# Performance work log

Measured on AMD Instinct MI355X. Metric: run time of the kernel, lower is better.

## Reference

```python
import jax, jax.numpy as jnp
import numpy as np

EMBED_DIM = 1024
NUM_HEADS = 8
HEAD_DIM = EMBED_DIM // NUM_HEADS


def setup_inputs() -> dict:
    key = jax.random.key(0)
    k1, k2, k3, k4, k5 = jax.random.split(key, 5)
    B, N, D = 4, 2048, EMBED_DIM
    scale = 1.0 / np.sqrt(D)
    return {
        "representation": jax.random.normal(k1, (B, N, D), dtype=jnp.float32),
        "W_qkv": jax.random.normal(k2, (D, 3 * D), dtype=jnp.float32) * scale,
        "b_qkv": jnp.zeros((3 * D,), dtype=jnp.float32),
        "W_proj": jax.random.normal(k3, (D, D), dtype=jnp.float32) * scale,
        "b_proj": jnp.zeros((D,), dtype=jnp.float32),
    }


def reference(representation, W_qkv, b_qkv, W_proj, b_proj):
    B, N, D = representation.shape
    H, Hd = NUM_HEADS, HEAD_DIM
    qkv = jnp.einsum("bnd,de->bne", representation, W_qkv) + b_qkv  # [B,N,3D]
    q, k, v = jnp.split(qkv, 3, axis=-1)
    # [B,N,D] -> [B,H,N,Hd]
    split_heads = lambda x: x.reshape(B, N, H, Hd).transpose(0, 2, 1, 3)
    q, k, v = split_heads(q), split_heads(k), split_heads(v)
    dots = jnp.einsum("bhqd,bhkd->bhqk", q, k) * (Hd ** -0.5)  # [B,H,N,N]
    attn = jax.nn.softmax(dots, axis=-1)
    out = jnp.einsum("bhqk,bhkd->bhqd", attn, v)
    out = out.transpose(0, 2, 1, 3).reshape(B, N, D)  # merge heads
    return jnp.einsum("bnd,de->bne", out, W_proj) + b_proj
```

## Files before the change

kernel.cpp:

```cpp
#include <hip/hip_runtime.h>
#include <hip/hip_bf16.h>
#include <cstdint>

typedef unsigned short u16;
typedef __attribute__((ext_vector_type(8))) short short8;
typedef __attribute__((ext_vector_type(4))) float f32x4;
typedef __attribute__((ext_vector_type(4))) unsigned short u16x4;
typedef __attribute__((ext_vector_type(4))) unsigned int u32x4;

#define NSEQ 2048
#define DMODEL 1024
#define NH 8
#define HD 128
#define KDIM 1024
#define QSCALE (0.08838834764831845f * 1.4426950408889634f)

__device__ __forceinline__ u16 f2b(float f) {
  __hip_bfloat16 h = __float2bfloat16(f);
  union { __hip_bfloat16 h; u16 u; } cv; cv.h = h; return cv.u;
}
__device__ __forceinline__ f32x4 zero4() { f32x4 z = {0.f, 0.f, 0.f, 0.f}; return z; }

__device__ __forceinline__ void gload_lds16(const u16* g, u16* l) {
  __builtin_amdgcn_global_load_lds(
      (__attribute__((address_space(1))) void*)g,
      (__attribute__((address_space(3))) void*)l, 16, 0, 0);
}

__device__ __forceinline__ int LK(int r) {
  return (r & 0x23) | ((r & 0x0C) << 1) | ((r & 0x10) >> 2);
}

__global__ void cvt_f32_bf16(const float* __restrict__ in, u16* __restrict__ out) {
  const size_t i = ((size_t)blockIdx.x * 256 + threadIdx.x) * 8;
  f32x4 a = *(const f32x4*)&in[i];
  f32x4 b = *(const f32x4*)&in[i + 4];
  short8 o;
#pragma unroll
  for (int j = 0; j < 4; ++j) { o[j] = (short)f2b(a[j]); o[4 + j] = (short)f2b(b[j]); }
  *(short8*)&out[i] = o;
}

__global__ void transpose_k(const float* __restrict__ in, u16* __restrict__ out,
                            int R, int C) {
  __shared__ u16 tile[32][33];
  const int tx = threadIdx.x, ty = threadIdx.y;
  const int c = blockIdx.x * 32 + tx;
  const int r0 = blockIdx.y * 32;
  for (int i = ty; i < 32; i += 8) tile[i][tx] = f2b(in[(size_t)(r0 + i) * C + c]);
  __syncthreads();
  const int oc = r0 + tx;
  const int c0 = blockIdx.x * 32;
  for (int i = ty; i < 32; i += 8) out[(size_t)(c0 + i) * R + oc] = tile[tx][i];
}

template <int MODE>
__global__ __launch_bounds__(512, 2) void gemm_pipe(
    const u16* __restrict__ A, const u16* __restrict__ Bt,
    const float* __restrict__ bias, u16* __restrict__ o0,
    u16* __restrict__ o1, u16* __restrict__ o2, float* __restrict__ of) {
  __shared__ __align__(16) u16 sA[2][256 * 64];
  __shared__ __align__(16) u16 sB[2][128 * 64];

  const int tid = threadIdx.x;
  const int lane = tid & 63;
  const int w = tid >> 6;
  const int quad = lane >> 4, ln = lane & 15;
  const int wm = w >> 1, wn = w & 1;

  const int NT = (MODE == 0) ? 24 : 8;
  const int nwg = gridDim.x, cpx = nwg >> 3;
  const int id = blockIdx.x;
  const int swz = (id & 7) * cpx + (id >> 3);
  const int m0 = (swz / NT) * 256, n0 = (swz % NT) * 128;

  const int r0 = tid >> 3, s0 = tid & 7;
  const u16* aSrc = A + (size_t)(m0 + r0) * KDIM + (s0 ^ (r0 & 7)) * 8;
  const u16* bSrc = Bt + (size_t)(n0 + r0) * KDIM + (s0 ^ (r0 & 7)) * 8;

  f32x4 acc[4][4];
#pragma unroll
  for (int i = 0; i < 4; ++i)
#pragma unroll
    for (int j = 0; j < 4; ++j) acc[i][j] = zero4();

  auto STAGE = [&](int ktn, int p) {
    u16* dA = &sA[ktn & 1][0];
    u16* dB = &sB[ktn & 1][0];
    const int k0n = ktn * 64;
    if (p == 0) {
      gload_lds16(aSrc + k0n,                        dA + tid * 8);
      gload_lds16(aSrc + (size_t)64 * KDIM + k0n,    dA + 64 * 64 + tid * 8);
      gload_lds16(aSrc + (size_t)128 * KDIM + k0n,   dA + 128 * 64 + tid * 8);
    } else {
      gload_lds16(aSrc + (size_t)192 * KDIM + k0n,   dA + 192 * 64 + tid * 8);
      gload_lds16(bSrc + k0n,                        dB + tid * 8);
      gload_lds16(bSrc + (size_t)64 * KDIM + k0n,    dB + 64 * 64 + tid * 8);
    }
  };

  STAGE(0, 0);
  STAGE(0, 1);

#pragma unroll 1
  for (int kt = 0; kt < KDIM / 64; ++kt) {
    const int bb = kt & 1;
    const u16* lA = &sA[bb][0];
    const u16* lB = &sB[bb][0];

    if (kt < KDIM / 64 - 1) {
      STAGE(kt + 1, 0);
      asm volatile("s_waitcnt vmcnt(3)" ::: "memory");
    } else {
      asm volatile("s_waitcnt vmcnt(0)" ::: "memory");
    }
    __builtin_amdgcn_s_barrier();
    asm volatile("" ::: "memory");

    short8 af[4][2], bf[2][2];
#pragma unroll
    for (int mf = 0; mf < 4; ++mf)
#pragma unroll
      for (int kk = 0; kk < 2; ++kk)
        af[mf][kk] = *(const short8*)&lA[(wm * 64 + mf * 16 + ln) * 64 +
                                         ((((kk << 2) | quad)) ^ (ln & 7)) * 8];
#pragma unroll
    for (int nf = 0; nf < 2; ++nf)
#pragma unroll
      for (int kk = 0; kk < 2; ++kk)
        bf[nf][kk] = *(const short8*)&lB[(wn * 64 + nf * 16 + ln) * 64 +
                                         ((((kk << 2) | quad)) ^ (ln & 7)) * 8];
    asm volatile("s_waitcnt lgkmcnt(0)" ::: "memory");
    __builtin_amdgcn_sched_barrier(0);
    __builtin_amdgcn_s_setprio(1);
#pragma unroll
    for (int kk = 0; kk < 2; ++kk)
#pragma unroll
      for (int mf = 0; mf < 4; ++mf)
#pragma unroll
        for (int nf = 0; nf < 2; ++nf)
          acc[mf][nf] = __builtin_amdgcn_mfma_f32_16x16x32_bf16(
              af[mf][kk], bf[nf][kk], acc[mf][nf], 0, 0, 0);
    __builtin_amdgcn_s_setprio(0);

    if (kt < KDIM / 64 - 1) STAGE(kt + 1, 1);
#pragma unroll
    for (int nf = 0; nf < 2; ++nf)
#pragma unroll
      for (int kk = 0; kk < 2; ++kk)
        bf[nf][kk] = *(const short8*)&lB[(wn * 64 + (nf + 2) * 16 + ln) * 64 +
                                         ((((kk << 2) | quad)) ^ (ln & 7)) * 8];
    asm volatile("s_waitcnt lgkmcnt(0)" ::: "memory");
    __builtin_amdgcn_sched_barrier(0);
    __builtin_amdgcn_s_setprio(1);
#pragma unroll
    for (int kk = 0; kk < 2; ++kk)
#pragma unroll
      for (int mf = 0; mf < 4; ++mf)
#pragma unroll
        for (int nf = 0; nf < 2; ++nf)
          acc[mf][nf + 2] = __builtin_amdgcn_mfma_f32_16x16x32_bf16(
              af[mf][kk], bf[nf][kk], acc[mf][nf + 2], 0, 0, 0);
    __builtin_amdgcn_s_setprio(0);
  }

  if (MODE == 0) {
    const int which = n0 >> 10;
    const int h = (n0 & 1023) >> 7;
#pragma unroll
    for (int mf = 0; mf < 4; ++mf) {
      const int rbase = m0 + wm * 64 + mf * 16 + quad * 4;
      const int b = rbase >> 11;
      const int n = rbase & 2047;
#pragma unroll
      for (int nf = 0; nf < 4; ++nf) {
        const int dcol = wn * 64 + nf * 16 + ln;
        const float bv = bias[n0 + dcol];
        if (which == 0) {
          u16* p = o0 + ((size_t)(b * NH + h) * NSEQ + n) * HD + dcol;
#pragma unroll
          for (int rr = 0; rr < 4; ++rr)
            p[(size_t)rr * HD] = f2b((acc[mf][nf][rr] + bv) * QSCALE);
        } else if (which == 1) {
          u16* p = o1 + ((size_t)(b * NH + h) * NSEQ + n) * HD + dcol;
#pragma unroll
          for (int rr = 0; rr < 4; ++rr)
            p[(size_t)rr * HD] = f2b(acc[mf][nf][rr] + bv);
        } else {
          u16x4 pk;
#pragma unroll
          for (int rr = 0; rr < 4; ++rr) pk[rr] = f2b(acc[mf][nf][rr] + bv);
          *(u16x4*)&o2[((size_t)(b * NH + h) * HD + dcol) * NSEQ + n] = pk;
        }
      }
    }
  } else {
#pragma unroll
    for (int mf = 0; mf < 4; ++mf) {
      const int rbase = m0 + wm * 64 + mf * 16 + quad * 4;
#pragma unroll
      for (int nf = 0; nf < 4; ++nf) {
        const int col = n0 + wn * 64 + nf * 16 + ln;
        const float bv = bias[col];
#pragma unroll
        for (int rr = 0; rr < 4; ++rr)
          of[(size_t)(rbase + rr) * DMODEL + col] = acc[mf][nf][rr] + bv;
      }
    }
  }
}

__global__ __launch_bounds__(256, 2) void attn_fused(
    const u16* __restrict__ Q, const u16* __restrict__ K,
    const u16* __restrict__ Vt, u16* __restrict__ AO) {
  __shared__ __align__(16) u16 sK[2][64 * 128];
  __shared__ __align__(16) u16 sV[2][128 * 64];

  const int tid = threadIdx.x;
  const int w = tid >> 6, lane = tid & 63;
  const int quad = lane >> 4, ln = lane & 15;
  const int bh = blockIdx.y;
  const int q0 = blockIdx.x * 128;

  const u16* Qb = Q + ((size_t)bh * NSEQ + q0) * HD;
  const u16* Kb = K + (size_t)bh * NSEQ * HD;
  const u16* Vb = Vt + (size_t)bh * HD * NSEQ;

  int gk_off[4], gv_off[4];
#pragma unroll
  for (int j = 0; j < 4; ++j) {
    const int c = (w * 4 + j) * 64 + lane;
    const int rk = c >> 4, sk_ = c & 15;
    gk_off[j] = LK(rk) * HD + (sk_ ^ (rk & 7)) * 8;
    const int rv = c >> 3, sv_ = c & 7;
    gv_off[j] = rv * NSEQ + (sv_ ^ (rv & 7)) * 8;
  }

  int kbase[4], kslot[4], vfo[2][8];
#pragma unroll
  for (int n = 0; n < 4; ++n) kbase[n] = (n * 16 + ln) * 128;
#pragma unroll
  for (int ks = 0; ks < 4; ++ks)
    kslot[ks] = (((ks << 2) | quad) ^ (ln & 7)) * 8;
#pragma unroll
  for (int ks2 = 0; ks2 < 2; ++ks2)
#pragma unroll
    for (int dt = 0; dt < 8; ++dt)
      vfo[ks2][dt] = (dt * 16 + ln) * 64 + ((((ks2 << 2) | quad) ^ (ln & 7)) * 8);

  short8 qf[2][4];
#pragma unroll
  for (int mt = 0; mt < 2; ++mt)
#pragma unroll
    for (int ks = 0; ks < 4; ++ks)
      qf[mt][ks] = *(const short8*)&Qb[(size_t)(w * 32 + mt * 16 + ln) * HD +
                                       ks * 32 + quad * 8];

  f32x4 o[2][8];
#pragma unroll
  for (int mt = 0; mt < 2; ++mt)
#pragma unroll
    for (int dt = 0; dt < 8; ++dt) o[mt][dt] = zero4();
  float l_part[2] = {0.f, 0.f};

#pragma unroll
  for (int j = 0; j < 4; ++j) {
    gload_lds16(Kb + gk_off[j], &sK[0][(w * 4 + j) * 512]);
    gload_lds16(Vb + gv_off[j], &sV[0][(w * 4 + j) * 512]);
  }

  union PU { u32x4 u; short8 s; };

#pragma unroll 1
  for (int it = 0; it < NSEQ / 128; ++it) {
#pragma unroll
    for (int c2 = 0; c2 < 2; ++c2) {
      __syncthreads();

      const int kvn = it * 128 + c2 * 64 + 64;
      if (kvn < NSEQ) {
#pragma unroll
        for (int j = 0; j < 4; ++j) {
          gload_lds16(Kb + (size_t)kvn * HD + gk_off[j],
                      &sK[c2 ^ 1][(w * 4 + j) * 512]);
          gload_lds16(Vb + kvn + gv_off[j], &sV[c2 ^ 1][(w * 4 + j) * 512]);
        }
      }
      const u16* skr = &sK[c2][0];
      const u16* svr = &sV[c2][0];

      __builtin_amdgcn_s_setprio(1);

      f32x4 sacc[4][2];
      PU ph[2][2];
      short8 vf0[8], vf1[8];

      auto SM = [&](int m) {
#pragma unroll
        for (int mt = 0; mt < 2; ++mt) {
          float e0 = exp2f(sacc[m][mt][0]);
          float e1 = exp2f(sacc[m][mt][1]);
          float e2 = exp2f(sacc[m][mt][2]);
          float e3 = exp2f(sacc[m][mt][3]);
          l_part[mt] += (e0 + e1) + (e2 + e3);
          unsigned a0 = __float_as_uint(e0) + 0x8000u;
          unsigned a1 = __float_as_uint(e1) + 0x8000u;
          unsigned a2 = __float_as_uint(e2) + 0x8000u;
          unsigned a3 = __float_as_uint(e3) + 0x8000u;
          ph[mt][m >> 1].u[(m & 1) * 2 + 0] = __builtin_amdgcn_perm(a1, a0, 0x07060302);
          ph[mt][m >> 1].u[(m & 1) * 2 + 1] = __builtin_amdgcn_perm(a3, a2, 0x07060302);
        }
      };

#pragma unroll
      for (int n = 0; n < 4; ++n) {
#pragma unroll
        for (int mt = 0; mt < 2; ++mt) sacc[n][mt] = zero4();
#pragma unroll
        for (int ks = 0; ks < 4; ++ks) {
          short8 kf = *(const short8*)&skr[kbase[n] + kslot[ks]];
          sacc[n][0] = __builtin_amdgcn_mfma_f32_16x16x32_bf16(
              kf, qf[0][ks], sacc[n][0], 0, 0, 0);
          sacc[n][1] = __builtin_amdgcn_mfma_f32_16x16x32_bf16(
              kf, qf[1][ks], sacc[n][1], 0, 0, 0);
        }
        if (n == 1) {
#pragma unroll
          for (int dt = 0; dt < 4; ++dt)
            vf0[dt] = *(const short8*)&svr[vfo[0][dt]];
        } else if (n == 2) {
#pragma unroll
          for (int dt = 4; dt < 8; ++dt)
            vf0[dt] = *(const short8*)&svr[vfo[0][dt]];
        }
        if (n) SM(n - 1);
      }

      {
        short8 pf0 = ph[0][0].s, pf1 = ph[1][0].s;
#pragma unroll
        for (int dt = 0; dt < 8; ++dt) {
          o[0][dt] = __builtin_amdgcn_mfma_f32_16x16x32_bf16(
              pf0, vf0[dt], o[0][dt], 0, 0, 0);
          o[1][dt] = __builtin_amdgcn_mfma_f32_16x16x32_bf16(
              pf1, vf0[dt], o[1][dt], 0, 0, 0);
        }
      }
#pragma unroll
      for (int dt = 0; dt < 8; ++dt)
        vf1[dt] = *(const short8*)&svr[vfo[1][dt]];
      SM(3);
      {
        short8 pf0 = ph[0][1].s, pf1 = ph[1][1].s;
#pragma unroll
        for (int dt = 0; dt < 8; ++dt) {
          o[0][dt] = __builtin_amdgcn_mfma_f32_16x16x32_bf16(
              pf0, vf1[dt], o[0][dt], 0, 0, 0);
          o[1][dt] = __builtin_amdgcn_mfma_f32_16x16x32_bf16(
              pf1, vf1[dt], o[1][dt], 0, 0, 0);
        }
      }
      __builtin_amdgcn_s_setprio(0);
    }
  }

  const int b = bh >> 3, h = bh & 7;
#pragma unroll
  for (int mt = 0; mt < 2; ++mt) {
    float v = l_part[mt];
    v += __shfl_xor(v, 16, 64);
    v += __shfl_xor(v, 32, 64);
    float inv[4];
#pragma unroll
    for (int rr = 0; rr < 4; ++rr)
      inv[rr] = 1.0f / __shfl(v, quad * 4 + rr, 64);
    const int rbase = q0 + w * 32 + mt * 16 + quad * 4;
#pragma unroll
    for (int dt = 0; dt < 8; ++dt) {
      const int d = dt * 16 + ln;
#pragma unroll
      for (int rr = 0; rr < 4; ++rr)
        AO[((size_t)b * NSEQ + rbase + rr) * DMODEL + h * HD + d] =
            f2b(o[mt][dt][rr] * inv[rr]);
    }
  }
}

extern "C" void kernel_launch(void* const* d_in, const int* in_sizes, int n_in,
                              void* d_out, int out_size, void* d_ws, size_t ws_size,
                              hipStream_t stream) {
  const float* X = (const float*)d_in[0];
  const float* Wqkv = (const float*)d_in[1];
  const float* bqkv = (const float*)d_in[2];
  const float* Wproj = (const float*)d_in[3];
  const float* bproj = (const float*)d_in[4];
  float* out = (float*)d_out;

  const size_t NEED_BYTES =
      2ull * (8388608  + 3072 * 1024 + 1024 * 1024 + 3 * 8388608 + 8388608);
  if (ws_size < NEED_BYTES) return;

  u16* ws = (u16*)d_ws;
  u16* Xb = ws;
  u16* WqkvT = Xb + 8388608;
  u16* WprojT = WqkvT + 3072 * 1024;
  u16* Qb = WprojT + 1024 * 1024;
  u16* Kb = Qb + 8388608;
  u16* Vtb = Kb + 8388608;
  u16* AO = Vtb + 8388608;

  cvt_f32_bf16<<<8388608 / (256 * 8), 256, 0, stream>>>(X, Xb);
  transpose_k<<<dim3(3072 / 32, 1024 / 32), dim3(32, 8), 0, stream>>>(Wqkv, WqkvT, 1024, 3072);
  transpose_k<<<dim3(1024 / 32, 1024 / 32), dim3(32, 8), 0, stream>>>(Wproj, WprojT, 1024, 1024);
  gemm_pipe<0><<<768, 512, 0, stream>>>(Xb, WqkvT, bqkv, Qb, Kb, Vtb, nullptr);
  attn_fused<<<dim3(2048 / 128, 32), 256, 0, stream>>>(Qb, Kb, Vtb, AO);
  gemm_pipe<1><<<256, 512, 0, stream>>>(AO, WprojT, bproj, nullptr, nullptr, nullptr, out);
}
```

Before: 269.8 us.

## Shrink GEMM tiles to 128x128 with 256-thread blocks and simpler staging

Replaces the 256x128 tile, 512-thread GEMM with a 128x128 tile on 256 threads (4 waves, each computing 64x64), doubling the grid size. The split two-phase prefetch is replaced by a single stage of 8 loads per k-step with an extra barrier before it. The goal is more workgroups for better CU fill and lower LDS per block. The cost is less operand reuse per tile, more global traffic, and a less interleaved load/compute schedule.

```diff
diff --git a/kernel.cpp b/kernel.cpp
--- a/kernel.cpp
+++ b/kernel.cpp
@@ -55,28 +55,34 @@
 }
 
 template <int MODE>
-__global__ __launch_bounds__(512, 2) void gemm_pipe(
+__global__ __launch_bounds__(256, 2) void gemm_pipe(
     const u16* __restrict__ A, const u16* __restrict__ Bt,
     const float* __restrict__ bias, u16* __restrict__ o0,
     u16* __restrict__ o1, u16* __restrict__ o2, float* __restrict__ of) {
-  __shared__ __align__(16) u16 sA[2][256 * 64];
+  __shared__ __align__(16) u16 sA[2][128 * 64];
   __shared__ __align__(16) u16 sB[2][128 * 64];
 
   const int tid = threadIdx.x;
   const int lane = tid & 63;
   const int w = tid >> 6;
   const int quad = lane >> 4, ln = lane & 15;
-  const int wm = w >> 1, wn = w & 1;
+  const int wm = (w >> 1) * 64, wn = (w & 1) * 64;
 
   const int NT = (MODE == 0) ? 24 : 8;
   const int nwg = gridDim.x, cpx = nwg >> 3;
   const int id = blockIdx.x;
   const int swz = (id & 7) * cpx + (id >> 3);
-  const int m0 = (swz / NT) * 256, n0 = (swz % NT) * 128;
-
-  const int r0 = tid >> 3, s0 = tid & 7;
-  const u16* aSrc = A + (size_t)(m0 + r0) * KDIM + (s0 ^ (r0 & 7)) * 8;
-  const u16* bSrc = Bt + (size_t)(n0 + r0) * KDIM + (s0 ^ (r0 & 7)) * 8;
+  const int m0 = (swz / NT) * 128, n0 = (swz % NT) * 128;
+
+  const int rr0 = tid >> 3, ss0 = tid & 7;
+  size_t a_off[4], b_off[4];
+#pragma unroll
+  for (int i = 0; i < 4; ++i) {
+    const int r = i * 32 + rr0;
+    const int so = (ss0 ^ (r & 7)) * 8;
+    a_off[i] = (size_t)(m0 + r) * KDIM + so;
+    b_off[i] = (size_t)(n0 + r) * KDIM + so;
+  }
 
   f32x4 acc[4][4];
 #pragma unroll
@@ -84,51 +90,47 @@
 #pragma unroll
     for (int j = 0; j < 4; ++j) acc[i][j] = zero4();
 
-  auto STAGE = [&](int ktn, int p) {
+  auto STAGE = [&](int ktn) {
     u16* dA = &sA[ktn & 1][0];
     u16* dB = &sB[ktn & 1][0];
     const int k0n = ktn * 64;
-    if (p == 0) {
-      gload_lds16(aSrc + k0n,                        dA + tid * 8);
-      gload_lds16(aSrc + (size_t)64 * KDIM + k0n,    dA + 64 * 64 + tid * 8);
-      gload_lds16(aSrc + (size_t)128 * KDIM + k0n,   dA + 128 * 64 + tid * 8);
-    } else {
-      gload_lds16(aSrc + (size_t)192 * KDIM + k0n,   dA + 192 * 64 + tid * 8);
-      gload_lds16(bSrc + k0n,                        dB + tid * 8);
-      gload_lds16(bSrc + (size_t)64 * KDIM + k0n,    dB + 64 * 64 + tid * 8);
+#pragma unroll
+    for (int i = 0; i < 4; ++i) {
+      gload_lds16(A + a_off[i] + k0n, dA + i * 2048 + tid * 8);
+      gload_lds16(Bt + b_off[i] + k0n, dB + i * 2048 + tid * 8);
     }
   };
 
-  STAGE(0, 0);
-  STAGE(0, 1);
+  STAGE(0);
 
 #pragma unroll 1
   for (int kt = 0; kt < KDIM / 64; ++kt) {
-    const int bb = kt & 1;
-    const u16* lA = &sA[bb][0];
-    const u16* lB = &sB[bb][0];
-
+    const u16* lA = &sA[kt & 1][0];
+    const u16* lB = &sB[kt & 1][0];
+
+    __builtin_amdgcn_s_barrier();
+    asm volatile("" ::: "memory");
     if (kt < KDIM / 64 - 1) {
-      STAGE(kt + 1, 0);
-      asm volatile("s_waitcnt vmcnt(3)" ::: "memory");
+      STAGE(kt + 1);
+      asm volatile("s_waitcnt vmcnt(8)" ::: "memory");
     } else {
       asm volatile("s_waitcnt vmcnt(0)" ::: "memory");
     }
     __builtin_amdgcn_s_barrier();
     asm volatile("" ::: "memory");
 
-    short8 af[4][2], bf[2][2];
+    short8 af[4][2], bf[4][2];
 #pragma unroll
     for (int mf = 0; mf < 4; ++mf)
 #pragma unroll
       for (int kk = 0; kk < 2; ++kk)
-        af[mf][kk] = *(const short8*)&lA[(wm * 64 + mf * 16 + ln) * 64 +
+        af[mf][kk] = *(const short8*)&lA[(wm + mf * 16 + ln) * 64 +
                                          ((((kk << 2) | quad)) ^ (ln & 7)) * 8];
 #pragma unroll
-    for (int nf = 0; nf < 2; ++nf)
+    for (int nf = 0; nf < 4; ++nf)
 #pragma unroll
       for (int kk = 0; kk < 2; ++kk)
-        bf[nf][kk] = *(const short8*)&lB[(wn * 64 + nf * 16 + ln) * 64 +
+        bf[nf][kk] = *(const short8*)&lB[(wn + nf * 16 + ln) * 64 +
                                          ((((kk << 2) | quad)) ^ (ln & 7)) * 8];
     asm volatile("s_waitcnt lgkmcnt(0)" ::: "memory");
     __builtin_amdgcn_sched_barrier(0);
@@ -138,30 +140,10 @@
 #pragma unroll
       for (int mf = 0; mf < 4; ++mf)
 #pragma unroll
-        for (int nf = 0; nf < 2; ++nf)
+        for (int nf = 0; nf < 4; ++nf)
           acc[mf][nf] = __builtin_amdgcn_mfma_f32_16x16x32_bf16(
               af[mf][kk], bf[nf][kk], acc[mf][nf], 0, 0, 0);
     __builtin_amdgcn_s_setprio(0);
-
-    if (kt < KDIM / 64 - 1) STAGE(kt + 1, 1);
-#pragma unroll
-    for (int nf = 0; nf < 2; ++nf)
-#pragma unroll
-      for (int kk = 0; kk < 2; ++kk)
-        bf[nf][kk] = *(const short8*)&lB[(wn * 64 + (nf + 2) * 16 + ln) * 64 +
-                                         ((((kk << 2) | quad)) ^ (ln & 7)) * 8];
-    asm volatile("s_waitcnt lgkmcnt(0)" ::: "memory");
-    __builtin_amdgcn_sched_barrier(0);
-    __builtin_amdgcn_s_setprio(1);
-#pragma unroll
-    for (int kk = 0; kk < 2; ++kk)
-#pragma unroll
-      for (int mf = 0; mf < 4; ++mf)
-#pragma unroll
-        for (int nf = 0; nf < 2; ++nf)
-          acc[mf][nf + 2] = __builtin_amdgcn_mfma_f32_16x16x32_bf16(
-              af[mf][kk], bf[nf][kk], acc[mf][nf + 2], 0, 0, 0);
-    __builtin_amdgcn_s_setprio(0);
   }
 
   if (MODE == 0) {
@@ -169,12 +151,12 @@
     const int h = (n0 & 1023) >> 7;
 #pragma unroll
     for (int mf = 0; mf < 4; ++mf) {
-      const int rbase = m0 + wm * 64 + mf * 16 + quad * 4;
+      const int rbase = m0 + wm + mf * 16 + quad * 4;
       const int b = rbase >> 11;
       const int n = rbase & 2047;
 #pragma unroll
       for (int nf = 0; nf < 4; ++nf) {
-        const int dcol = wn * 64 + nf * 16 + ln;
+        const int dcol = wn + nf * 16 + ln;
         const float bv = bias[n0 + dcol];
         if (which == 0) {
           u16* p = o0 + ((size_t)(b * NH + h) * NSEQ + n) * HD + dcol;
@@ -197,10 +179,10 @@
   } else {
 #pragma unroll
     for (int mf = 0; mf < 4; ++mf) {
-      const int rbase = m0 + wm * 64 + mf * 16 + quad * 4;
+      const int rbase = m0 + wm + mf * 16 + quad * 4;
 #pragma unroll
       for (int nf = 0; nf < 4; ++nf) {
-        const int col = n0 + wn * 64 + nf * 16 + ln;
+        const int col = n0 + wn + nf * 16 + ln;
         const float bv = bias[col];
 #pragma unroll
         for (int rr = 0; rr < 4; ++rr)
@@ -412,7 +394,7 @@
   cvt_f32_bf16<<<8388608 / (256 * 8), 256, 0, stream>>>(X, Xb);
   transpose_k<<<dim3(3072 / 32, 1024 / 32), dim3(32, 8), 0, stream>>>(Wqkv, WqkvT, 1024, 3072);
   transpose_k<<<dim3(1024 / 32, 1024 / 32), dim3(32, 8), 0, stream>>>(Wproj, WprojT, 1024, 1024);
-  gemm_pipe<0><<<768, 512, 0, stream>>>(Xb, WqkvT, bqkv, Qb, Kb, Vtb, nullptr);
+  gemm_pipe<0><<<1536, 256, 0, stream>>>(Xb, WqkvT, bqkv, Qb, Kb, Vtb, nullptr);
   attn_fused<<<dim3(2048 / 128, 32), 256, 0, stream>>>(Qb, Kb, Vtb, AO);
-  gemm_pipe<1><<<256, 512, 0, stream>>>(AO, WprojT, bproj, nullptr, nullptr, nullptr, out);
-}
+  gemm_pipe<1><<<512, 256, 0, stream>>>(AO, WprojT, bproj, nullptr, nullptr, nullptr, out);
+}
```

New measurement: 267.7 us. About the same (-0.8%).
